# Kernel tuning notes

Measured on AMD Instinct MI355X. Metric: run time of the kernel, lower is better.

Reference implementation:

```python
import jax, jax.numpy as jnp
import numpy as np
from jax import lax

B, T, I, H = 128, 512, 300, 256


def setup_inputs() -> dict:
    key = jax.random.key(0)
    ks = jax.random.split(key, 10)
    k = 1.0 / np.sqrt(H)
    u = lambda kk, shape: jax.random.uniform(kk, shape, jnp.float32, -k, k)
    return {
        "x": jax.random.normal(ks[0], (B, T, I), jnp.float32),
        "W_ih_f": u(ks[1], (4 * H, I)),
        "W_hh_f": u(ks[2], (4 * H, H)),
        "b_f": u(ks[3], (4 * H,)),
        "W_ih_b": u(ks[4], (4 * H, I)),
        "W_hh_b": u(ks[5], (4 * H, H)),
        "b_b": u(ks[6], (4 * H,)),
        "W_lin": u(ks[7], (2, 2 * H)),
        "b_lin": u(ks[8], (2,)),
    }


def _lstm_dir(x, W_ih, W_hh, b, reverse):
    # Precompute input projections for all timesteps: [B, T, 4H]
    xp = jnp.einsum("bti,gi->btg", x, W_ih) + b
    if reverse:
        xp = xp[:, ::-1]
    h0 = jnp.zeros((x.shape[0], H), x.dtype)
    c0 = jnp.zeros((x.shape[0], H), x.dtype)

    def step(carry, xt):
        h, c = carry
        g = xt + h @ W_hh.T  # [B, 4H]
        i_g, f_g, g_g, o_g = jnp.split(g, 4, axis=-1)  # torch gate order i,f,g,o
        i_g = jax.nn.sigmoid(i_g)
        f_g = jax.nn.sigmoid(f_g)
        g_g = jnp.tanh(g_g)
        o_g = jax.nn.sigmoid(o_g)
        c = f_g * c + i_g * g_g
        h = o_g * jnp.tanh(c)
        return (h, c), h

    _, hs = lax.scan(step, (h0, c0), jnp.swapaxes(xp, 0, 1))  # [T, B, H]
    hs = jnp.swapaxes(hs, 0, 1)  # [B, T, H]
    if reverse:
        hs = hs[:, ::-1]
    return hs


def reference(x, W_ih_f, W_hh_f, b_f, W_ih_b, W_hh_b, b_b, W_lin, b_lin):
    hf = _lstm_dir(x, W_ih_f, W_hh_f, b_f, reverse=False)  # [B, T, H]
    hb = _lstm_dir(x, W_ih_b, W_hh_b, b_b, reverse=True)   # [B, T, H]
    last = jnp.concatenate([hf[:, -1], hb[:, -1]], axis=-1)  # [B, 2H]
    return last @ W_lin.T + b_lin  # [B, 2]
```

## Files before the change

### kernel.cpp

```cpp
#include <hip/hip_runtime.h>
#include <cstdint>
#include <cstddef>

typedef _Float16 half2v __attribute__((ext_vector_type(2)));
typedef _Float16 half4v __attribute__((ext_vector_type(4)));
typedef _Float16 half8v __attribute__((ext_vector_type(8)));
typedef float f32x4 __attribute__((ext_vector_type(4)));

#if __has_builtin(__builtin_amdgcn_fdot2)
#define FDOT2(a, b, c) __builtin_amdgcn_fdot2((a), (b), (c), false)
#else
static __device__ __forceinline__ float fdot2_fb(half2v a, half2v b, float c) {
    return c + (float)a[0] * (float)b[0] + (float)a[1] * (float)b[1];
}
#define FDOT2(a, b, c) fdot2_fb((a), (b), (c))
#endif

__device__ __forceinline__ float sigm(float x) { return 1.0f / (1.0f + __expf(-x)); }
__device__ __forceinline__ float tanh_(float x) { return 1.0f - 2.0f / (__expf(2.0f * x) + 1.0f); }

#define BB 128
#define TT 512
#define II 300
#define HH 256
#define GG 1024

__global__ __launch_bounds__(256, 3) void gemm_xp(
    const float* __restrict__ X, const float* __restrict__ W,
    const float* __restrict__ bias, _Float16* __restrict__ XP)
{
    __shared__ _Float16 As[128 * 32];
    __shared__ _Float16 Bs[128 * 32];

    const int t = threadIdx.x;
    const int m0 = blockIdx.y * 128;
    const int n0 = blockIdx.x * 128;
    const int kpos = t & 7;
    const int rbase = t >> 3;
    const int lane = t & 63;
    const int wv = t >> 6;
    const int mq = (wv >> 1) * 4;
    const int nq = (wv & 1) * 4;

    f32x4 acc[4][4];
#pragma unroll
    for (int i = 0; i < 4; ++i)
#pragma unroll
        for (int j = 0; j < 4; ++j) acc[i][j] = f32x4{0.f, 0.f, 0.f, 0.f};

    for (int kc = 0; kc < 320; kc += 32) {
        __syncthreads();
        const int k0 = kc + kpos * 4;
#pragma unroll
        for (int rr = 0; rr < 4; ++rr) {
            const int row = rbase + rr * 32;
            float4 va = {0.f, 0.f, 0.f, 0.f}, vb = {0.f, 0.f, 0.f, 0.f};
            if (k0 < 300) {
                va = *(const float4*)(X + (size_t)(m0 + row) * II + k0);
                vb = *(const float4*)(W + (size_t)(n0 + row) * II + k0);
            }
            const int idx = (row >> 4) * 512 + (kpos >> 1) * 128 + (row & 15) * 8 + (kpos & 1) * 4;
            half4v ha = {(_Float16)va.x, (_Float16)va.y, (_Float16)va.z, (_Float16)va.w};
            half4v hb = {(_Float16)vb.x, (_Float16)vb.y, (_Float16)vb.z, (_Float16)vb.w};
            *(half4v*)(&As[idx]) = ha;
            *(half4v*)(&Bs[idx]) = hb;
        }
        __syncthreads();

        half8v af[4], bf[4];
#pragma unroll
        for (int i = 0; i < 4; ++i) {
            af[i] = *(const half8v*)(&As[(mq + i) * 512 + (lane >> 4) * 128 + (lane & 15) * 8]);
            bf[i] = *(const half8v*)(&Bs[(nq + i) * 512 + (lane >> 4) * 128 + (lane & 15) * 8]);
        }
#pragma unroll
        for (int i = 0; i < 4; ++i)
#pragma unroll
            for (int j = 0; j < 4; ++j)
                acc[i][j] = __builtin_amdgcn_mfma_f32_16x16x32_f16(af[i], bf[j], acc[i][j], 0, 0, 0);
    }

#pragma unroll
    for (int j = 0; j < 4; ++j) {
        const int n = n0 + (nq + j) * 16 + (lane & 15);
        const float bv = bias[n];
#pragma unroll
        for (int i = 0; i < 4; ++i) {
#pragma unroll
            for (int r = 0; r < 4; ++r) {
                const int m = m0 + (mq + i) * 16 + (lane >> 4) * 4 + r;
                XP[(size_t)m * GG + n] = (_Float16)(acc[i][j][r] + bv);
            }
        }
    }
}

__global__ __attribute__((amdgpu_flat_work_group_size(512, 512), amdgpu_waves_per_eu(2, 2)))
void lstm_fwd(
    const float* __restrict__ Whh, const _Float16* __restrict__ XP,
    float* __restrict__ HF)
{
    __shared__ _Float16 wlds[8 * GG * 8];
    __shared__ __align__(16) _Float16 hlds[2][HH];

    const int t = threadIdx.x;
    const int b = blockIdx.x;
    const int l = t & 63;
    const int wv = t >> 6;
    const int half = l >> 5;
    const int j = wv * 32 + (l & 31);
    const int row0 = j + (half ? 256 : 0);
    const int row1 = row0 + 512;

    half2v w0[96], w1[96];
#pragma unroll
    for (int i = 0; i < 48; ++i) {
        float4 v = *(const float4*)(Whh + (size_t)row0 * HH + i * 4);
        w0[2 * i]     = half2v{(_Float16)v.x, (_Float16)v.y};
        w0[2 * i + 1] = half2v{(_Float16)v.z, (_Float16)v.w};
    }
#pragma unroll
    for (int i = 0; i < 48; ++i) {
        float4 v = *(const float4*)(Whh + (size_t)row1 * HH + i * 4);
        w1[2 * i]     = half2v{(_Float16)v.x, (_Float16)v.y};
        w1[2 * i + 1] = half2v{(_Float16)v.z, (_Float16)v.w};
    }
#pragma unroll
    for (int grp = 0; grp < 8; ++grp) {
        float4 a  = *(const float4*)(Whh + (size_t)t * HH + 192 + grp * 8);
        float4 c4 = *(const float4*)(Whh + (size_t)t * HH + 192 + grp * 8 + 4);
        half8v hv = {(_Float16)a.x, (_Float16)a.y, (_Float16)a.z, (_Float16)a.w,
                     (_Float16)c4.x, (_Float16)c4.y, (_Float16)c4.z, (_Float16)c4.w};
        *(half8v*)(&wlds[grp * (GG * 8) + t * 8]) = hv;
        float4 a2 = *(const float4*)(Whh + (size_t)(t + 512) * HH + 192 + grp * 8);
        float4 c2 = *(const float4*)(Whh + (size_t)(t + 512) * HH + 192 + grp * 8 + 4);
        half8v hv2 = {(_Float16)a2.x, (_Float16)a2.y, (_Float16)a2.z, (_Float16)a2.w,
                      (_Float16)c2.x, (_Float16)c2.y, (_Float16)c2.z, (_Float16)c2.w};
        *(half8v*)(&wlds[grp * (GG * 8) + (t + 512) * 8]) = hv2;
    }
    if (t < HH) hlds[0][t] = (_Float16)0.f;
    float c = 0.0f;
    __syncthreads();

    const _Float16* xp_b = XP + (size_t)b * TT * GG;
    _Float16 x0 = xp_b[row0];
    _Float16 x1 = xp_b[row1];

    for (int ts = 0; ts < TT; ++ts) {
        const int p = ts & 1;
        const _Float16* hrd = &hlds[p][0];
        const _Float16* xp_n = xp_b + ((ts < TT - 1) ? GG : 0);
        const _Float16 nx0 = xp_n[row0];
        const _Float16 nx1 = xp_n[row1];

        float a0 = 0.f, a1 = 0.f;
#pragma unroll
        for (int cq = 0; cq < 24; ++cq) {
            half8v hv = *(const half8v*)(&hrd[cq * 8]);
            half2v h0 = __builtin_shufflevector(hv, hv, 0, 1);
            half2v h1 = __builtin_shufflevector(hv, hv, 2, 3);
            half2v h2 = __builtin_shufflevector(hv, hv, 4, 5);
            half2v h3 = __builtin_shufflevector(hv, hv, 6, 7);
            a0 = FDOT2(h0, w0[cq * 4 + 0], a0);
            a1 = FDOT2(h0, w1[cq * 4 + 0], a1);
            a0 = FDOT2(h1, w0[cq * 4 + 1], a0);
            a1 = FDOT2(h1, w1[cq * 4 + 1], a1);
            a0 = FDOT2(h2, w0[cq * 4 + 2], a0);
            a1 = FDOT2(h2, w1[cq * 4 + 2], a1);
            a0 = FDOT2(h3, w0[cq * 4 + 3], a0);
            a1 = FDOT2(h3, w1[cq * 4 + 3], a1);
        }
#define LDS_W_STEP(I0, I1)                                                 \
        {                                                                  \
            half2v hp  = __builtin_shufflevector(hv, hv, I0, I1);          \
            half2v wap = __builtin_shufflevector(wa, wa, I0, I1);          \
            half2v wbp = __builtin_shufflevector(wb, wb, I0, I1);          \
            a0 = FDOT2(hp, wap, a0);                                       \
            a1 = FDOT2(hp, wbp, a1);                                       \
        }
#pragma unroll
        for (int grp = 0; grp < 8; ++grp) {
            half8v hv = *(const half8v*)(&hrd[192 + grp * 8]);
            half8v wa = *(const half8v*)(&wlds[grp * (GG * 8) + row0 * 8]);
            half8v wb = *(const half8v*)(&wlds[grp * (GG * 8) + row1 * 8]);
            LDS_W_STEP(0, 1)
            LDS_W_STEP(2, 3)
            LDS_W_STEP(4, 5)
            LDS_W_STEP(6, 7)
        }
#undef LDS_W_STEP
        const float o0 = a0 + (float)x0;
        const float o1 = a1 + (float)x1;
        const float p0 = __shfl_xor(o0, 32, 64);
        const float p1 = __shfl_xor(o1, 32, 64);
        const float gi = half ? p0 : o0;
        const float gg = half ? p1 : o1;
        const float gf = half ? o0 : p0;
        const float go = half ? o1 : p1;
        c = sigm(gf) * c + sigm(gi) * tanh_(gg);
        const float h = sigm(go) * tanh_(c);
        if (!half) {
            hlds[p ^ 1][j] = (_Float16)h;
            if (ts == TT - 1) HF[(size_t)b * HH + j] = h;
        }
        __syncthreads();

        x0 = nx0;
        x1 = nx1;
        xp_b = xp_n;
    }
}

__global__ __launch_bounds__(256) void lstm_bwd(
    const float* __restrict__ X, const float* __restrict__ Wih,
    const float* __restrict__ bb, float* __restrict__ HB)
{
    __shared__ float xs[II];
    const int b = blockIdx.x, t = threadIdx.x;
    const float* xrow = X + ((size_t)b * TT + (TT - 1)) * II;
    if (t < 75) *(float4*)(&xs[t * 4]) = *(const float4*)(xrow + t * 4);
    __syncthreads();
    if (t < HH) {
        float ai = 0.f, ag = 0.f, ao = 0.f;
        const float4* wi = (const float4*)(Wih + (size_t)t * II);
        const float4* wg = (const float4*)(Wih + (size_t)(t + 512) * II);
        const float4* wo = (const float4*)(Wih + (size_t)(t + 768) * II);
        for (int k4 = 0; k4 < 75; ++k4) {
            float4 xv = *(const float4*)(&xs[k4 * 4]);
            float4 a = wi[k4], g4 = wg[k4], o4 = wo[k4];
            ai += xv.x * a.x + xv.y * a.y + xv.z * a.z + xv.w * a.w;
            ag += xv.x * g4.x + xv.y * g4.y + xv.z * g4.z + xv.w * g4.w;
            ao += xv.x * o4.x + xv.y * o4.y + xv.z * o4.z + xv.w * o4.w;
        }
        ai += bb[t];
        ag += bb[t + 512];
        ao += bb[t + 768];
        const float cg = sigm(ai) * tanh_(ag);
        HB[(size_t)b * HH + t] = sigm(ao) * tanh_(cg);
    }
}

__global__ __launch_bounds__(256) void final_k(
    const float* __restrict__ HF, const float* __restrict__ HB,
    const float* __restrict__ Wlin, const float* __restrict__ blin,
    float* __restrict__ OUT)
{
    const int t = threadIdx.x;
    const int b = t >> 1, jj = t & 1;
    float acc = blin[jj];
    const float* wf = Wlin + jj * 512;
    const float* wb = Wlin + jj * 512 + 256;
    const float* hf = HF + (size_t)b * HH;
    const float* hb = HB + (size_t)b * HH;
    for (int k = 0; k < HH; k += 4) {
        float4 h4 = *(const float4*)(hf + k);
        float4 w4 = *(const float4*)(wf + k);
        float4 g4 = *(const float4*)(hb + k);
        float4 v4 = *(const float4*)(wb + k);
        acc += h4.x * w4.x + h4.y * w4.y + h4.z * w4.z + h4.w * w4.w;
        acc += g4.x * v4.x + g4.y * v4.y + g4.z * v4.z + g4.w * v4.w;
    }
    OUT[b * 2 + jj] = acc;
}

extern "C" void kernel_launch(void* const* d_in, const int* in_sizes, int n_in,
                              void* d_out, int out_size, void* d_ws, size_t ws_size,
                              hipStream_t stream)
{
    const float* x = (const float*)d_in[0];
    const float* Wihf = (const float*)d_in[1];
    const float* Whhf = (const float*)d_in[2];
    const float* bf = (const float*)d_in[3];
    const float* Wihb = (const float*)d_in[4];
    const float* Whhb = (const float*)d_in[5];
    const float* bbv = (const float*)d_in[6];
    const float* Wlin = (const float*)d_in[7];
    const float* blin = (const float*)d_in[8];
    float* out = (float*)d_out;
    (void)Whhb; (void)in_sizes; (void)n_in; (void)out_size; (void)ws_size;

    _Float16* xp = (_Float16*)d_ws;
    float* hf = (float*)((char*)d_ws + (size_t)BB * TT * GG * 2);
    float* hb = hf + (size_t)BB * HH;

    lstm_bwd<<<BB, 256, 0, stream>>>(x, Wihb, bbv, hb);
    gemm_xp<<<dim3(GG / 128, (BB * TT) / 128), 256, 0, stream>>>(x, Wihf, bf, xp);
    lstm_fwd<<<BB, 512, 0, stream>>>(Whhf, xp, hf);
    final_k<<<1, 256, 0, stream>>>(hf, hb, Wlin, blin, out);
}
```

Baseline: 1.320 ms.

## Split LSTM recurrent matvec across K lanes with permlane swap reductions

Restructures the forward LSTM recurrence so each lane covers a 64-wide slice of the hidden dimension for 8 gate rows, not all 256 columns for 2 rows. Partial sums are combined with permlane16/32 swap reductions, and the hidden state is written to four padded copies in LDS to spread bank accesses. Each lane now computes all four gates directly, removing the old cross-half gate exchange. This cuts per-lane serial dot-product length and LDS broadcast reads, at the cost of cross-lane reduction work each timestep and more LDS writes.

```diff
diff --git a/kernel.cpp b/kernel.cpp
--- a/kernel.cpp
+++ b/kernel.cpp
@@ -6,6 +6,7 @@
 typedef _Float16 half4v __attribute__((ext_vector_type(4)));
 typedef _Float16 half8v __attribute__((ext_vector_type(8)));
 typedef float f32x4 __attribute__((ext_vector_type(4)));
+typedef unsigned int uint2v __attribute__((ext_vector_type(2)));
 
 #if __has_builtin(__builtin_amdgcn_fdot2)
 #define FDOT2(a, b, c) __builtin_amdgcn_fdot2((a), (b), (c), false)
@@ -18,6 +19,23 @@
 
 __device__ __forceinline__ float sigm(float x) { return 1.0f / (1.0f + __expf(-x)); }
 __device__ __forceinline__ float tanh_(float x) { return 1.0f - 2.0f / (__expf(2.0f * x) + 1.0f); }
+
+static __device__ __forceinline__ float xred16(float x) {
+#if __has_builtin(__builtin_amdgcn_permlane16_swap)
+    uint2v r = __builtin_amdgcn_permlane16_swap(__float_as_uint(x), __float_as_uint(x), false, false);
+    return __uint_as_float(r[0]) + __uint_as_float(r[1]);
+#else
+    return x + __shfl_xor(x, 16, 64);
+#endif
+}
+static __device__ __forceinline__ float xred32(float x) {
+#if __has_builtin(__builtin_amdgcn_permlane32_swap)
+    uint2v r = __builtin_amdgcn_permlane32_swap(__float_as_uint(x), __float_as_uint(x), false, false);
+    return __uint_as_float(r[0]) + __uint_as_float(r[1]);
+#else
+    return x + __shfl_xor(x, 32, 64);
+#endif
+}
 
 #define BB 128
 #define TT 512
@@ -100,113 +118,124 @@
     const float* __restrict__ Whh, const _Float16* __restrict__ XP,
     float* __restrict__ HF)
 {
-    __shared__ _Float16 wlds[8 * GG * 8];
-    __shared__ __align__(16) _Float16 hlds[2][HH];
+    __shared__ _Float16 wlds[16 * 512 * 8];
+    __shared__ __align__(16) _Float16 hbuf[2][1056];
 
     const int t = threadIdx.x;
     const int b = blockIdx.x;
     const int l = t & 63;
     const int wv = t >> 6;
-    const int half = l >> 5;
+    const int m = l & 15;
+    const int g = (l >> 4) & 3;
+    const bool rowev = ((l >> 4) & 1) == 0;
     const int j = wv * 32 + (l & 31);
-    const int row0 = j + (half ? 256 : 0);
-    const int row1 = row0 + 512;
-
-    half2v w0[96], w1[96];
-#pragma unroll
-    for (int i = 0; i < 48; ++i) {
-        float4 v = *(const float4*)(Whh + (size_t)row0 * HH + i * 4);
-        w0[2 * i]     = half2v{(_Float16)v.x, (_Float16)v.y};
-        w0[2 * i + 1] = half2v{(_Float16)v.z, (_Float16)v.w};
-    }
-#pragma unroll
-    for (int i = 0; i < 48; ++i) {
-        float4 v = *(const float4*)(Whh + (size_t)row1 * HH + i * 4);
-        w1[2 * i]     = half2v{(_Float16)v.x, (_Float16)v.y};
-        w1[2 * i + 1] = half2v{(_Float16)v.z, (_Float16)v.w};
-    }
-#pragma unroll
-    for (int grp = 0; grp < 8; ++grp) {
-        float4 a  = *(const float4*)(Whh + (size_t)t * HH + 192 + grp * 8);
-        float4 c4 = *(const float4*)(Whh + (size_t)t * HH + 192 + grp * 8 + 4);
-        half8v hv = {(_Float16)a.x, (_Float16)a.y, (_Float16)a.z, (_Float16)a.w,
-                     (_Float16)c4.x, (_Float16)c4.y, (_Float16)c4.z, (_Float16)c4.w};
-        *(half8v*)(&wlds[grp * (GG * 8) + t * 8]) = hv;
-        float4 a2 = *(const float4*)(Whh + (size_t)(t + 512) * HH + 192 + grp * 8);
-        float4 c2 = *(const float4*)(Whh + (size_t)(t + 512) * HH + 192 + grp * 8 + 4);
-        half8v hv2 = {(_Float16)a2.x, (_Float16)a2.y, (_Float16)a2.z, (_Float16)a2.w,
-                      (_Float16)c2.x, (_Float16)c2.y, (_Float16)c2.z, (_Float16)c2.w};
-        *(half8v*)(&wlds[grp * (GG * 8) + (t + 512) * 8]) = hv2;
-    }
-    if (t < HH) hlds[0][t] = (_Float16)0.f;
+    const int ja = wv * 32 + m;
+    const int kbase = g * 64;
+
+    int rows[8];
+    rows[0] = ja;       rows[1] = ja + 256; rows[2] = ja + 512; rows[3] = ja + 768;
+    rows[4] = ja + 16;  rows[5] = ja + 272; rows[6] = ja + 528; rows[7] = ja + 784;
+
+    half2v w[8][24];
+#pragma unroll
+    for (int r = 0; r < 8; ++r) {
+        const float* wr = Whh + (size_t)rows[r] * HH + kbase;
+#pragma unroll
+        for (int i4 = 0; i4 < 12; ++i4) {
+            float4 v = *(const float4*)(wr + i4 * 4);
+            w[r][i4 * 2]     = half2v{(_Float16)v.x, (_Float16)v.y};
+            w[r][i4 * 2 + 1] = half2v{(_Float16)v.z, (_Float16)v.w};
+        }
+#pragma unroll
+        for (int cc = 0; cc < 2; ++cc) {
+            float4 a  = *(const float4*)(wr + 48 + cc * 8);
+            float4 b4 = *(const float4*)(wr + 48 + cc * 8 + 4);
+            half8v hv = {(_Float16)a.x,  (_Float16)a.y,  (_Float16)a.z,  (_Float16)a.w,
+                         (_Float16)b4.x, (_Float16)b4.y, (_Float16)b4.z, (_Float16)b4.w};
+            *(half8v*)(&wlds[(r * 2 + cc) * 4096 + t * 8]) = hv;
+        }
+    }
+    if (t < 256) {
+        hbuf[0][t]       = (_Float16)0.f;
+        hbuf[0][264 + t] = (_Float16)0.f;
+        hbuf[0][528 + t] = (_Float16)0.f;
+        hbuf[0][792 + t] = (_Float16)0.f;
+    }
     float c = 0.0f;
     __syncthreads();
 
-    const _Float16* xp_b = XP + (size_t)b * TT * GG;
-    _Float16 x0 = xp_b[row0];
-    _Float16 x1 = xp_b[row1];
+    const _Float16* xp_b = XP + (size_t)b * TT * GG + j;
+    _Float16 x0 = xp_b[0], x1 = xp_b[256], x2 = xp_b[512], x3 = xp_b[768];
+
+    const int hoff = g * 328;
 
     for (int ts = 0; ts < TT; ++ts) {
         const int p = ts & 1;
-        const _Float16* hrd = &hlds[p][0];
+        const _Float16* hrd = &hbuf[p][hoff];
         const _Float16* xp_n = xp_b + ((ts < TT - 1) ? GG : 0);
-        const _Float16 nx0 = xp_n[row0];
-        const _Float16 nx1 = xp_n[row1];
-
-        float a0 = 0.f, a1 = 0.f;
-#pragma unroll
-        for (int cq = 0; cq < 24; ++cq) {
-            half8v hv = *(const half8v*)(&hrd[cq * 8]);
+        const _Float16 nx0 = xp_n[0], nx1 = xp_n[256], nx2 = xp_n[512], nx3 = xp_n[768];
+
+        float s[8] = {0.f, 0.f, 0.f, 0.f, 0.f, 0.f, 0.f, 0.f};
+#pragma unroll
+        for (int ch = 0; ch < 6; ++ch) {
+            half8v hv = *(const half8v*)(hrd + ch * 8);
             half2v h0 = __builtin_shufflevector(hv, hv, 0, 1);
             half2v h1 = __builtin_shufflevector(hv, hv, 2, 3);
             half2v h2 = __builtin_shufflevector(hv, hv, 4, 5);
             half2v h3 = __builtin_shufflevector(hv, hv, 6, 7);
-            a0 = FDOT2(h0, w0[cq * 4 + 0], a0);
-            a1 = FDOT2(h0, w1[cq * 4 + 0], a1);
-            a0 = FDOT2(h1, w0[cq * 4 + 1], a0);
-            a1 = FDOT2(h1, w1[cq * 4 + 1], a1);
-            a0 = FDOT2(h2, w0[cq * 4 + 2], a0);
-            a1 = FDOT2(h2, w1[cq * 4 + 2], a1);
-            a0 = FDOT2(h3, w0[cq * 4 + 3], a0);
-            a1 = FDOT2(h3, w1[cq * 4 + 3], a1);
-        }
-#define LDS_W_STEP(I0, I1)                                                 \
-        {                                                                  \
-            half2v hp  = __builtin_shufflevector(hv, hv, I0, I1);          \
-            half2v wap = __builtin_shufflevector(wa, wa, I0, I1);          \
-            half2v wbp = __builtin_shufflevector(wb, wb, I0, I1);          \
-            a0 = FDOT2(hp, wap, a0);                                       \
-            a1 = FDOT2(hp, wbp, a1);                                       \
-        }
-#pragma unroll
-        for (int grp = 0; grp < 8; ++grp) {
-            half8v hv = *(const half8v*)(&hrd[192 + grp * 8]);
-            half8v wa = *(const half8v*)(&wlds[grp * (GG * 8) + row0 * 8]);
-            half8v wb = *(const half8v*)(&wlds[grp * (GG * 8) + row1 * 8]);
-            LDS_W_STEP(0, 1)
-            LDS_W_STEP(2, 3)
-            LDS_W_STEP(4, 5)
-            LDS_W_STEP(6, 7)
-        }
-#undef LDS_W_STEP
-        const float o0 = a0 + (float)x0;
-        const float o1 = a1 + (float)x1;
-        const float p0 = __shfl_xor(o0, 32, 64);
-        const float p1 = __shfl_xor(o1, 32, 64);
-        const float gi = half ? p0 : o0;
-        const float gg = half ? p1 : o1;
-        const float gf = half ? o0 : p0;
-        const float go = half ? o1 : p1;
-        c = sigm(gf) * c + sigm(gi) * tanh_(gg);
+#pragma unroll
+            for (int r = 0; r < 8; ++r) {
+                s[r] = FDOT2(h0, w[r][ch * 4 + 0], s[r]);
+                s[r] = FDOT2(h1, w[r][ch * 4 + 1], s[r]);
+                s[r] = FDOT2(h2, w[r][ch * 4 + 2], s[r]);
+                s[r] = FDOT2(h3, w[r][ch * 4 + 3], s[r]);
+            }
+        }
+#pragma unroll
+        for (int cc = 0; cc < 2; ++cc) {
+            half8v hv = *(const half8v*)(hrd + (6 + cc) * 8);
+            half2v h0 = __builtin_shufflevector(hv, hv, 0, 1);
+            half2v h1 = __builtin_shufflevector(hv, hv, 2, 3);
+            half2v h2 = __builtin_shufflevector(hv, hv, 4, 5);
+            half2v h3 = __builtin_shufflevector(hv, hv, 6, 7);
+#pragma unroll
+            for (int r = 0; r < 8; ++r) {
+                half8v wl = *(const half8v*)(&wlds[(r * 2 + cc) * 4096 + t * 8]);
+                half2v q0 = __builtin_shufflevector(wl, wl, 0, 1);
+                half2v q1 = __builtin_shufflevector(wl, wl, 2, 3);
+                half2v q2 = __builtin_shufflevector(wl, wl, 4, 5);
+                half2v q3 = __builtin_shufflevector(wl, wl, 6, 7);
+                s[r] = FDOT2(h0, q0, s[r]);
+                s[r] = FDOT2(h1, q1, s[r]);
+                s[r] = FDOT2(h2, q2, s[r]);
+                s[r] = FDOT2(h3, q3, s[r]);
+            }
+        }
+
+        const float t0 = xred16(s[0]), t1 = xred16(s[1]), t2 = xred16(s[2]), t3 = xred16(s[3]);
+        const float t4 = xred16(s[4]), t5 = xred16(s[5]), t6 = xred16(s[6]), t7 = xred16(s[7]);
+        float vi = rowev ? t0 : t4;
+        float vf = rowev ? t1 : t5;
+        float vg = rowev ? t2 : t6;
+        float vo = rowev ? t3 : t7;
+        vi = xred32(vi); vf = xred32(vf); vg = xred32(vg); vo = xred32(vo);
+
+        const float gi = vi + (float)x0;
+        const float gf = vf + (float)x1;
+        const float gG = vg + (float)x2;
+        const float go = vo + (float)x3;
+        c = sigm(gf) * c + sigm(gi) * tanh_(gG);
         const float h = sigm(go) * tanh_(c);
-        if (!half) {
-            hlds[p ^ 1][j] = (_Float16)h;
-            if (ts == TT - 1) HF[(size_t)b * HH + j] = h;
-        }
+
+        _Float16* hw = &hbuf[p ^ 1][0];
+        const int cp = (l < 32) ? 0 : 528;
+        const _Float16 hh = (_Float16)h;
+        hw[cp + j] = hh;
+        hw[cp + 264 + j] = hh;
+        if (ts == TT - 1 && l < 32) HF[(size_t)b * HH + j] = h;
         __syncthreads();
 
-        x0 = nx0;
-        x1 = nx1;
+        x0 = nx0; x1 = nx1; x2 = nx2; x3 = nx3;
         xp_b = xp_n;
     }
 }
```

Measured after the change: 1.450 ms. 1.1x slower.

## Pre-convert X and W_ih to padded fp16 and use direct-to-LDS loads in GEMM

Applied to the files above, without the earlier changes.

Adds a conversion kernel that writes X and the forward W_ih as fp16 with K padded to 320. A new GEMM then streams these tiles straight into LDS with global_load_lds and 16x16x32 MFMA. The aim is to remove the fp32-to-fp16 conversion and register staging from the GEMM's inner loop and to halve the bytes the GEMM reads. In exchange it adds an extra pass over X, needs extra workspace (with a fallback when that is short), and the GEMM has no double buffering.

```diff
diff --git a/kernel.cpp b/kernel.cpp
--- a/kernel.cpp
+++ b/kernel.cpp
@@ -22,8 +22,129 @@
 #define BB 128
 #define TT 512
 #define II 300
+#define IIP 320
 #define HH 256
 #define GG 1024
+
+__global__ __launch_bounds__(256) void cvt_xw(
+    const float* __restrict__ X, const float* __restrict__ W,
+    _Float16* __restrict__ Xh, _Float16* __restrict__ Wh)
+{
+    const int total = (65536 + 1024) * 40;
+    for (int c = blockIdx.x * 256 + threadIdx.x; c < total; c += gridDim.x * 256) {
+        const int row = c / 40;
+        const int ch = c - row * 40;
+        const int k0 = ch * 8;
+        const float* src;
+        _Float16* dst;
+        if (row < 65536) {
+            src = X + (size_t)row * II;
+            dst = Xh + (size_t)row * IIP;
+        } else {
+            src = W + (size_t)(row - 65536) * II;
+            dst = Wh + (size_t)(row - 65536) * IIP;
+        }
+        half8v hv;
+        if (k0 + 8 <= II) {
+            float4 a = *(const float4*)(src + k0);
+            float4 b = *(const float4*)(src + k0 + 4);
+            hv = half8v{(_Float16)a.x, (_Float16)a.y, (_Float16)a.z, (_Float16)a.w,
+                        (_Float16)b.x, (_Float16)b.y, (_Float16)b.z, (_Float16)b.w};
+        } else {
+#pragma unroll
+            for (int q = 0; q < 8; ++q) {
+                const int k = k0 + q;
+                hv[q] = (k < II) ? (_Float16)src[k] : (_Float16)0.f;
+            }
+        }
+        *(half8v*)(dst + k0) = hv;
+    }
+}
+
+#if __has_builtin(__builtin_amdgcn_global_load_lds)
+#define HAVE_GLL 1
+__device__ __forceinline__ void gll16(const _Float16* g, _Float16* l) {
+    __builtin_amdgcn_global_load_lds(
+        (const __attribute__((address_space(1))) void*)g,
+        (__attribute__((address_space(3))) void*)l, 16, 0, 0);
+}
+#else
+#define HAVE_GLL 0
+#endif
+
+__global__ __launch_bounds__(256) void gemm_xp_h(
+    const _Float16* __restrict__ Xh, const _Float16* __restrict__ Wh,
+    const float* __restrict__ bias, _Float16* __restrict__ XP)
+{
+    __shared__ __align__(16) _Float16 As[128 * 32];
+    __shared__ __align__(16) _Float16 Bs[128 * 32];
+
+    const int t = threadIdx.x;
+    const int m0 = blockIdx.y * 128;
+    const int n0 = blockIdx.x * 128;
+    const int lane = t & 63;
+    const int wv = t >> 6;
+    const int mq = (wv >> 1) * 4;
+    const int nq = (wv & 1) * 4;
+
+    int rowd[2], k4d[2], cidx[2];
+#pragma unroll
+    for (int r = 0; r < 2; ++r) {
+        const int c = wv * 128 + r * 64 + lane;
+        cidx[r] = c;
+        rowd[r] = ((c >> 6) << 4) | (c & 15);
+        k4d[r] = (c >> 4) & 3;
+    }
+
+    f32x4 acc[4][4];
+#pragma unroll
+    for (int i = 0; i < 4; ++i)
+#pragma unroll
+        for (int j = 0; j < 4; ++j) acc[i][j] = f32x4{0.f, 0.f, 0.f, 0.f};
+
+    for (int kc = 0; kc < IIP; kc += 32) {
+        __syncthreads();
+#pragma unroll
+        for (int r = 0; r < 2; ++r) {
+            const _Float16* ga = Xh + (size_t)(m0 + rowd[r]) * IIP + kc + k4d[r] * 8;
+            const _Float16* gb = Wh + (size_t)(n0 + rowd[r]) * IIP + kc + k4d[r] * 8;
+#if HAVE_GLL
+            gll16(ga, &As[cidx[r] * 8]);
+            gll16(gb, &Bs[cidx[r] * 8]);
+#else
+            *(half8v*)(&As[cidx[r] * 8]) = *(const half8v*)ga;
+            *(half8v*)(&Bs[cidx[r] * 8]) = *(const half8v*)gb;
+#endif
+        }
+        __syncthreads();
+
+        half8v af[4], bf[4];
+#pragma unroll
+        for (int i = 0; i < 4; ++i) {
+            af[i] = *(const half8v*)(&As[(mq + i) * 512 + (lane >> 4) * 128 + (lane & 15) * 8]);
+            bf[i] = *(const half8v*)(&Bs[(nq + i) * 512 + (lane >> 4) * 128 + (lane & 15) * 8]);
+        }
+#pragma unroll
+        for (int i = 0; i < 4; ++i)
+#pragma unroll
+            for (int j = 0; j < 4; ++j)
+                acc[i][j] = __builtin_amdgcn_mfma_f32_16x16x32_f16(af[i], bf[j], acc[i][j], 0, 0, 0);
+    }
+
+#pragma unroll
+    for (int j = 0; j < 4; ++j) {
+        const int n = n0 + (nq + j) * 16 + (lane & 15);
+        const float bv = bias[n];
+#pragma unroll
+        for (int i = 0; i < 4; ++i) {
+#pragma unroll
+            for (int r = 0; r < 4; ++r) {
+                const int m = m0 + (mq + i) * 16 + (lane >> 4) * 4 + r;
+                XP[(size_t)m * GG + n] = (_Float16)(acc[i][j][r] + bv);
+            }
+        }
+    }
+}
 
 __global__ __launch_bounds__(256, 3) void gemm_xp(
     const float* __restrict__ X, const float* __restrict__ W,
@@ -277,14 +398,26 @@
     const float* Wlin = (const float*)d_in[7];
     const float* blin = (const float*)d_in[8];
     float* out = (float*)d_out;
-    (void)Whhb; (void)in_sizes; (void)n_in; (void)out_size; (void)ws_size;
+    (void)Whhb; (void)in_sizes; (void)n_in; (void)out_size;
+
+    const size_t XP_B = (size_t)BB * TT * GG * 2;
+    const size_t H_B  = (size_t)BB * HH * 4;
+    const size_t XH_B = (size_t)65536 * IIP * 2;
+    const size_t WH_B = (size_t)GG * IIP * 2;
 
     _Float16* xp = (_Float16*)d_ws;
-    float* hf = (float*)((char*)d_ws + (size_t)BB * TT * GG * 2);
+    float* hf = (float*)((char*)d_ws + XP_B);
     float* hb = hf + (size_t)BB * HH;
+    _Float16* Xh = (_Float16*)((char*)d_ws + XP_B + 2 * H_B);
+    _Float16* Wh = Xh + (size_t)65536 * IIP;
 
     lstm_bwd<<<BB, 256, 0, stream>>>(x, Wihb, bbv, hb);
-    gemm_xp<<<dim3(GG / 128, (BB * TT) / 128), 256, 0, stream>>>(x, Wihf, bf, xp);
+    if (ws_size >= XP_B + 2 * H_B + XH_B + WH_B) {
+        cvt_xw<<<2048, 256, 0, stream>>>(x, Wihf, Xh, Wh);
+        gemm_xp_h<<<dim3(GG / 128, (BB * TT) / 128), 256, 0, stream>>>(Xh, Wh, bf, xp);
+    } else {
+        gemm_xp<<<dim3(GG / 128, (BB * TT) / 128), 256, 0, stream>>>(x, Wihf, bf, xp);
+    }
     lstm_fwd<<<BB, 512, 0, stream>>>(Whhf, xp, hf);
     final_k<<<1, 256, 0, stream>>>(hf, hb, Wlin, blin, out);
 }
```

Result: faster. 1.241 ms (-5.9%).
